# Performance work log

Measured on AMD Instinct MI355X. Metric: run time of the kernel, lower is better.

Reference implementation:

```python
import jax, jax.numpy as jnp
import numpy as np
from jax import lax

T = 5        # unrolled ISTA iterations (module default)
LAM = 0.1    # soft-threshold level (module default)
B, L, K = 4096, 4096, 128


def _conv1d_same(x, k):
    """TF-style SAME cross-correlation. x: [B, L], k: [K] -> [B, L]."""
    Kw = k.shape[0]
    pad_left = (Kw - 1) // 2
    pad_right = Kw - 1 - pad_left
    out = lax.conv_general_dilated(
        x[:, None, :],            # [B, 1, L]
        k[None, None, :],         # [O=1, I=1, K]
        window_strides=(1,),
        padding=[(pad_left, pad_right)],
        dimension_numbers=("NCH", "OIH", "NCH"),
    )
    return out[:, 0, :]


def setup_inputs() -> dict:
    key = jax.random.key(0)
    k1, k2 = jax.random.split(key)
    y = jax.random.normal(k1, (B, L), dtype=jnp.float32)
    thz_pulse = jax.random.normal(k2, (K,), dtype=jnp.float32)  # learned pulse (trainable)
    step_size = jnp.full((1,), 0.1, dtype=jnp.float32)          # learned step (trainable)
    return {"y": y, "thz_pulse": thz_pulse, "step_size": step_size}


def reference(y, thz_pulse, step_size):
    x = jnp.zeros_like(y)
    h = thz_pulse           # matched-filter kernel
    h_rev = thz_pulse[::-1] # time-reversed kernel (adjoint / correlation)
    s = step_size[0]
    for _ in range(T):
        conv_out = _conv1d_same(y, h)           # H y
        residual = y - conv_out                 # y - H y
        update = _conv1d_same(residual, h_rev)  # H^T residual
        x = x + s * update                      # gradient step
        x = jnp.sign(x) * jax.nn.relu(jnp.abs(x) - LAM)  # soft-threshold
    return x
```

## Files before the change

### kernel.cpp

```cpp
#include <hip/hip_runtime.h>


typedef __bf16 bf16;
typedef __bf16 bf16x4 __attribute__((ext_vector_type(4)));
typedef __bf16 bf16x8 __attribute__((ext_vector_type(8)));
typedef float f32x4 __attribute__((ext_vector_type(4)));

#define LC 512
#define PY 824
#define PR 664
#define LAM 0.1f

__global__ __launch_bounds__(256) void ista_mfma(
    const float* __restrict__ y, const float* __restrict__ h,
    const float* __restrict__ step, float* __restrict__ out) {
  __shared__ __align__(16) bf16 ys[16 * PY];
  __shared__ __align__(16) bf16 rs[16 * PR];
  __shared__ float hs[128];

  const int tid = threadIdx.x;
  const int lane = tid & 63;
  const int wave = tid >> 6;
  const int li = lane & 15;
  const int quad = lane >> 4;
  const int chunk0 = blockIdx.x * LC;
  const int b0 = blockIdx.y * 16;

  if (tid < 128) hs[tid] = h[tid];

  {
    const int rr = tid >> 4;
    const int t = tid & 15;
    const float* yrow = y + (size_t)(b0 + rr) * 4096;
    bf16* dst = ys + rr * PY;
    for (int s4 = t; s4 < 200; s4 += 16) {
      int l = chunk0 - 128 + s4 * 4;
      float4 v;
      if (l >= 0 && l <= 4096 - 4) {
        v = *reinterpret_cast<const float4*>(yrow + l);
      } else {
        v.x = (l + 0 >= 0 && l + 0 < 4096) ? yrow[l + 0] : 0.f;
        v.y = (l + 1 >= 0 && l + 1 < 4096) ? yrow[l + 1] : 0.f;
        v.z = (l + 2 >= 0 && l + 2 < 4096) ? yrow[l + 2] : 0.f;
        v.w = (l + 3 >= 0 && l + 3 < 4096) ? yrow[l + 3] : 0.f;
      }
      bf16x4 bv;
      bv[0] = (bf16)v.x; bv[1] = (bf16)v.y; bv[2] = (bf16)v.z; bv[3] = (bf16)v.w;
      *reinterpret_cast<bf16x4*>(dst + s4 * 4) = bv;
    }
  }
  __syncthreads();

  bf16x8 A1[5], A2[5];
#pragma unroll
  for (int dd = 0; dd < 5; ++dd) {
    int d = (dd - 2) * 32;
    bf16x8 a1, a2;
#pragma unroll
    for (int j = 0; j < 8; ++j) {
      int k = quad * 8 + j;
      int idx1 = 63 + d + k - li;
      a1[j] = (idx1 >= 0 && idx1 < 128) ? (bf16)hs[idx1] : (bf16)0.f;
      int idx2 = 64 + li - d - k;
      a2[j] = (idx2 >= 0 && idx2 < 128) ? (bf16)(-hs[idx2]) : (bf16)0.f;
    }
    A1[dd] = a1; A2[dd] = a2;
  }

  for (int t = wave; t < 41; t += 4) {
    int i0 = -64 + 16 * t;
    f32x4 acc;
    {
      bf16x4 yv = *reinterpret_cast<const bf16x4*>(
          ys + li * PY + (i0 + 128) + quad * 4);
      acc[0] = -(float)yv[0]; acc[1] = -(float)yv[1];
      acc[2] = -(float)yv[2]; acc[3] = -(float)yv[3];
    }
#pragma unroll
    for (int dd = 0; dd < 5; ++dd) {
      int d = (dd - 2) * 32;
      bf16x8 bfrag = *reinterpret_cast<const bf16x8*>(
          ys + li * PY + (i0 + d + 128) + quad * 8);
      acc = __builtin_amdgcn_mfma_f32_16x16x32_bf16(A1[dd], bfrag, acc, 0, 0, 0);
    }
    bf16x4 rv;
#pragma unroll
    for (int e = 0; e < 4; ++e) {
      int g = chunk0 + i0 + quad * 4 + e;
      float v = (g >= 0 && g < 4096) ? acc[e] : 0.f;
      rv[e] = (bf16)v;
    }
    *reinterpret_cast<bf16x4*>(rs + li * PR + (i0 + 64) + quad * 4) = rv;
  }
  __syncthreads();

  const float s = step[0];
  for (int t = wave; t < 32; t += 4) {
    int i0 = 16 * t;
    f32x4 acc = {0.f, 0.f, 0.f, 0.f};
#pragma unroll
    for (int dd = 0; dd < 5; ++dd) {
      int d = (dd - 2) * 32;
      bf16x8 bfrag = *reinterpret_cast<const bf16x8*>(
          rs + li * PR + (i0 + d + 64) + quad * 8);
      acc = __builtin_amdgcn_mfma_f32_16x16x32_bf16(A2[dd], bfrag, acc, 0, 0, 0);
    }
    float4 xv;
#pragma unroll
    for (int e = 0; e < 4; ++e) {
      float su = s * acc[e];
      float x = 0.f;
#pragma unroll
      for (int it = 0; it < 5; ++it) {
        x += su;
        float ax = fabsf(x) - LAM;
        ax = ax > 0.f ? ax : 0.f;
        x = copysignf(ax, x);
      }
      (&xv.x)[e] = x;
    }
    *reinterpret_cast<float4*>(
        out + (size_t)(b0 + li) * 4096 + chunk0 + i0 + quad * 4) = xv;
  }
}

extern "C" void kernel_launch(void* const* d_in, const int* in_sizes, int n_in,
                              void* d_out, int out_size, void* d_ws,
                              size_t ws_size, hipStream_t stream) {
  const float* y = (const float*)d_in[0];
  const float* h = (const float*)d_in[1];
  const float* s = (const float*)d_in[2];
  float* out = (float*)d_out;
  ista_mfma<<<dim3(4096 / LC, 256), dim3(256), 0, stream>>>(y, h, s, out);
}
```

Measured before the change: 142.2 us.

## Fold two convolutions into one composite kernel and close-form the soft-threshold loop

```diff
diff --git a/kernel.cpp b/kernel.cpp
--- a/kernel.cpp
+++ b/kernel.cpp
@@ -7,117 +7,228 @@
 typedef float f32x4 __attribute__((ext_vector_type(4)));
 
 #define LC 512
-#define PY 824
-#define PR 664
+#define PY 792
 #define LAM 0.1f
 
-__global__ __launch_bounds__(256) void ista_mfma(
+__global__ __launch_bounds__(256) void ista_g(
     const float* __restrict__ y, const float* __restrict__ h,
     const float* __restrict__ step, float* __restrict__ out) {
   __shared__ __align__(16) bf16 ys[16 * PY];
-  __shared__ __align__(16) bf16 rs[16 * PR];
-  __shared__ float hs[128];
+  __shared__ __align__(16) bf16 gpad[384];
+  __shared__ float hs[256];
 
   const int tid = threadIdx.x;
   const int lane = tid & 63;
-  const int wave = tid >> 6;
   const int li = lane & 15;
   const int quad = lane >> 4;
-  const int chunk0 = blockIdx.x * LC;
-  const int b0 = blockIdx.y * 16;
-
-  if (tid < 128) hs[tid] = h[tid];
+  const int wave = tid >> 6;
+  const int bid = blockIdx.x;
+  const int chunk0 = (bid >> 8) * LC;
+  const int b0 = (bid & 255) * 16;
+
+  {
+    float hv = 0.f;
+    if (tid < 128) hv = h[tid];
+    hs[tid] = hv;
+  }
 
   {
     const int rr = tid >> 4;
     const int t = tid & 15;
     const float* yrow = y + (size_t)(b0 + rr) * 4096;
     bf16* dst = ys + rr * PY;
-    for (int s4 = t; s4 < 200; s4 += 16) {
-      int l = chunk0 - 128 + s4 * 4;
-      float4 v;
-      if (l >= 0 && l <= 4096 - 4) {
-        v = *reinterpret_cast<const float4*>(yrow + l);
-      } else {
-        v.x = (l + 0 >= 0 && l + 0 < 4096) ? yrow[l + 0] : 0.f;
-        v.y = (l + 1 >= 0 && l + 1 < 4096) ? yrow[l + 1] : 0.f;
-        v.z = (l + 2 >= 0 && l + 2 < 4096) ? yrow[l + 2] : 0.f;
-        v.w = (l + 3 >= 0 && l + 3 < 4096) ? yrow[l + 3] : 0.f;
+#pragma unroll
+    for (int k = 0; k < 13; ++k) {
+      int s4 = t + 16 * k;
+      if (s4 < 196) {
+        int l = chunk0 - 128 + s4 * 4;
+        float4 v;
+        if (l >= 0 && l <= 4096 - 4) {
+          v = *reinterpret_cast<const float4*>(yrow + l);
+        } else {
+          v.x = ((unsigned)(l + 0) < 4096u) ? yrow[l + 0] : 0.f;
+          v.y = ((unsigned)(l + 1) < 4096u) ? yrow[l + 1] : 0.f;
+          v.z = ((unsigned)(l + 2) < 4096u) ? yrow[l + 2] : 0.f;
+          v.w = ((unsigned)(l + 3) < 4096u) ? yrow[l + 3] : 0.f;
+        }
+        bf16x4 bv;
+        bv[0] = (bf16)v.x; bv[1] = (bf16)v.y; bv[2] = (bf16)v.z; bv[3] = (bf16)v.w;
+        *reinterpret_cast<bf16x4*>(dst + s4 * 4) = bv;
       }
-      bf16x4 bv;
-      bv[0] = (bf16)v.x; bv[1] = (bf16)v.y; bv[2] = (bf16)v.z; bv[3] = (bf16)v.w;
-      *reinterpret_cast<bf16x4*>(dst + s4 * 4) = bv;
+    }
+  }
+  __syncthreads();
+
+  if (tid < 128) {
+    const int tau = tid;
+    float ac = 0.f;
+#pragma unroll 8
+    for (int m = 0; m < 128; ++m) ac += hs[m] * hs[m + tau];
+    float g1 = (tau <= 63) ? hs[63 - tau] : 0.f;
+    gpad[145 + tau] = (bf16)(g1 - ac);
+    if (tau > 0) {
+      float g2 = (tau <= 64) ? hs[63 + tau] : 0.f;
+      gpad[145 - tau] = (bf16)(g2 - ac);
+    }
+  } else {
+    const int r = tid - 128;
+    if (r < 18) gpad[r] = (bf16)0.f;
+    if (273 + r < 384) gpad[273 + r] = (bf16)0.f;
+  }
+  __syncthreads();
+
+  bf16x8 AG[9];
+  {
+    const int off = 144 + quad * 8 - li;
+#pragma unroll
+    for (int dd = 0; dd < 9; ++dd) {
+      bf16x8 a;
+      const int o = off + (dd - 4) * 32;
+#pragma unroll
+      for (int j = 0; j < 8; ++j) a[j] = gpad[o + j];
+      AG[dd] = a;
+    }
+  }
+
+  const float s = step[0];
+  for (int t = wave; t < 32; t += 4) {
+    const int i0 = 16 * t;
+    f32x4 acc0 = {0.f, 0.f, 0.f, 0.f};
+    f32x4 acc1 = {0.f, 0.f, 0.f, 0.f};
+    const bf16* brow = ys + li * PY + (i0 + 128) + quad * 8;
+#pragma unroll
+    for (int dd = 0; dd < 9; dd += 2) {
+      bf16x8 b = *reinterpret_cast<const bf16x8*>(brow + (dd - 4) * 32);
+      acc0 = __builtin_amdgcn_mfma_f32_16x16x32_bf16(AG[dd], b, acc0, 0, 0, 0);
+    }
+#pragma unroll
+    for (int dd = 1; dd < 9; dd += 2) {
+      bf16x8 b = *reinterpret_cast<const bf16x8*>(brow + (dd - 4) * 32);
+      acc1 = __builtin_amdgcn_mfma_f32_16x16x32_bf16(AG[dd], b, acc1, 0, 0, 0);
+    }
+    float4 xv;
+#pragma unroll
+    for (int e = 0; e < 4; ++e) {
+      float su = s * (acc0[e] + acc1[e]);
+      float ax = fabsf(su) - LAM;
+      ax = ax > 0.f ? ax : 0.f;
+      (&xv.x)[e] = 5.f * copysignf(ax, su);
+    }
+    *reinterpret_cast<float4*>(
+        out + (size_t)(b0 + li) * 4096 + chunk0 + i0 + quad * 4) = xv;
+  }
+}
+
+#define EC 64
+#define PYE 360
+#define PRE 216
+__global__ __launch_bounds__(256) void ista_edge(
+    const float* __restrict__ y, const float* __restrict__ h,
+    const float* __restrict__ step, float* __restrict__ out) {
+  __shared__ __align__(16) bf16 ys[16 * PYE];
+  __shared__ __align__(16) bf16 rs[16 * PRE];
+  __shared__ __align__(16) bf16 h1p[256], h2p[256];
+
+  const int tid = threadIdx.x;
+  const int lane = tid & 63;
+  const int li = lane & 15;
+  const int quad = lane >> 4;
+  const int wave = tid >> 6;
+  const int bid = blockIdx.x;
+  const int chunk0 = (bid & 1) ? (4096 - EC) : 0;
+  const int b0 = (bid >> 1) * 16;
+
+  {
+    const int p = tid;
+    int i1 = p - 64;
+    h1p[p] = ((unsigned)i1 < 128u) ? (bf16)h[i1] : (bf16)0.f;
+    int i2 = 191 - p;
+    h2p[p] = ((unsigned)i2 < 128u) ? (bf16)(-h[i2]) : (bf16)0.f;
+  }
+
+  {
+    const int rr = tid >> 4;
+    const int t = tid & 15;
+    const float* yrow = y + (size_t)(b0 + rr) * 4096;
+    bf16* dst = ys + rr * PYE;
+#pragma unroll
+    for (int k = 0; k < 6; ++k) {
+      int s4 = t + 16 * k;
+      if (s4 < 88) {
+        int l = chunk0 - 128 + s4 * 4;
+        float4 v;
+        if (l >= 0 && l <= 4096 - 4) {
+          v = *reinterpret_cast<const float4*>(yrow + l);
+        } else {
+          v.x = ((unsigned)(l + 0) < 4096u) ? yrow[l + 0] : 0.f;
+          v.y = ((unsigned)(l + 1) < 4096u) ? yrow[l + 1] : 0.f;
+          v.z = ((unsigned)(l + 2) < 4096u) ? yrow[l + 2] : 0.f;
+          v.w = ((unsigned)(l + 3) < 4096u) ? yrow[l + 3] : 0.f;
+        }
+        bf16x4 bv;
+        bv[0] = (bf16)v.x; bv[1] = (bf16)v.y; bv[2] = (bf16)v.z; bv[3] = (bf16)v.w;
+        *reinterpret_cast<bf16x4*>(dst + s4 * 4) = bv;
+      }
     }
   }
   __syncthreads();
 
   bf16x8 A1[5], A2[5];
-#pragma unroll
-  for (int dd = 0; dd < 5; ++dd) {
-    int d = (dd - 2) * 32;
-    bf16x8 a1, a2;
-#pragma unroll
-    for (int j = 0; j < 8; ++j) {
-      int k = quad * 8 + j;
-      int idx1 = 63 + d + k - li;
-      a1[j] = (idx1 >= 0 && idx1 < 128) ? (bf16)hs[idx1] : (bf16)0.f;
-      int idx2 = 64 + li - d - k;
-      a2[j] = (idx2 >= 0 && idx2 < 128) ? (bf16)(-hs[idx2]) : (bf16)0.f;
-    }
-    A1[dd] = a1; A2[dd] = a2;
-  }
-
-  for (int t = wave; t < 41; t += 4) {
-    int i0 = -64 + 16 * t;
+  {
+    const int off = 127 + quad * 8 - li;
+#pragma unroll
+    for (int dd = 0; dd < 5; ++dd) {
+      const int o = off + (dd - 2) * 32;
+      bf16x8 a1, a2;
+#pragma unroll
+      for (int j = 0; j < 8; ++j) { a1[j] = h1p[o + j]; a2[j] = h2p[o + j]; }
+      A1[dd] = a1; A2[dd] = a2;
+    }
+  }
+
+  for (int t = wave; t < 13; t += 4) {
+    const int i0 = -64 + 16 * t;
     f32x4 acc;
     {
       bf16x4 yv = *reinterpret_cast<const bf16x4*>(
-          ys + li * PY + (i0 + 128) + quad * 4);
+          ys + li * PYE + (i0 + 128) + quad * 4);
       acc[0] = -(float)yv[0]; acc[1] = -(float)yv[1];
       acc[2] = -(float)yv[2]; acc[3] = -(float)yv[3];
     }
 #pragma unroll
     for (int dd = 0; dd < 5; ++dd) {
-      int d = (dd - 2) * 32;
-      bf16x8 bfrag = *reinterpret_cast<const bf16x8*>(
-          ys + li * PY + (i0 + d + 128) + quad * 8);
-      acc = __builtin_amdgcn_mfma_f32_16x16x32_bf16(A1[dd], bfrag, acc, 0, 0, 0);
+      bf16x8 b = *reinterpret_cast<const bf16x8*>(
+          ys + li * PYE + (i0 + (dd - 2) * 32 + 128) + quad * 8);
+      acc = __builtin_amdgcn_mfma_f32_16x16x32_bf16(A1[dd], b, acc, 0, 0, 0);
     }
     bf16x4 rv;
 #pragma unroll
     for (int e = 0; e < 4; ++e) {
       int g = chunk0 + i0 + quad * 4 + e;
-      float v = (g >= 0 && g < 4096) ? acc[e] : 0.f;
+      float v = ((unsigned)g < 4096u) ? acc[e] : 0.f;
       rv[e] = (bf16)v;
     }
-    *reinterpret_cast<bf16x4*>(rs + li * PR + (i0 + 64) + quad * 4) = rv;
+    *reinterpret_cast<bf16x4*>(rs + li * PRE + (i0 + 64) + quad * 4) = rv;
   }
   __syncthreads();
 
   const float s = step[0];
-  for (int t = wave; t < 32; t += 4) {
-    int i0 = 16 * t;
+  for (int t = wave; t < 4; t += 4) {
+    const int i0 = 16 * t;
     f32x4 acc = {0.f, 0.f, 0.f, 0.f};
 #pragma unroll
     for (int dd = 0; dd < 5; ++dd) {
-      int d = (dd - 2) * 32;
-      bf16x8 bfrag = *reinterpret_cast<const bf16x8*>(
-          rs + li * PR + (i0 + d + 64) + quad * 8);
-      acc = __builtin_amdgcn_mfma_f32_16x16x32_bf16(A2[dd], bfrag, acc, 0, 0, 0);
+      bf16x8 b = *reinterpret_cast<const bf16x8*>(
+          rs + li * PRE + (i0 + (dd - 2) * 32 + 64) + quad * 8);
+      acc = __builtin_amdgcn_mfma_f32_16x16x32_bf16(A2[dd], b, acc, 0, 0, 0);
     }
     float4 xv;
 #pragma unroll
     for (int e = 0; e < 4; ++e) {
       float su = s * acc[e];
-      float x = 0.f;
-#pragma unroll
-      for (int it = 0; it < 5; ++it) {
-        x += su;
-        float ax = fabsf(x) - LAM;
-        ax = ax > 0.f ? ax : 0.f;
-        x = copysignf(ax, x);
-      }
-      (&xv.x)[e] = x;
+      float ax = fabsf(su) - LAM;
+      ax = ax > 0.f ? ax : 0.f;
+      (&xv.x)[e] = 5.f * copysignf(ax, su);
     }
     *reinterpret_cast<float4*>(
         out + (size_t)(b0 + li) * 4096 + chunk0 + i0 + quad * 4) = xv;
@@ -131,5 +242,6 @@
   const float* h = (const float*)d_in[1];
   const float* s = (const float*)d_in[2];
   float* out = (float*)d_out;
-  ista_mfma<<<dim3(4096 / LC, 256), dim3(256), 0, stream>>>(y, h, s, out);
+  ista_g<<<dim3(8 * 256), dim3(256), 0, stream>>>(y, h, s, out);
+  ista_edge<<<dim3(2 * 256), dim3(256), 0, stream>>>(y, h, s, out);
 }
```

New measurement: 149.3 us. 5.0% more time.
